# Optimization experiments

Hardware: AMD Instinct MI355X
Metric: run time of the kernel (lower is better)

## Reference

```python
import jax, jax.numpy as jnp
import numpy as np

NUM_GAUSSIANS = 3  # coordinate dims per spot; nfeatures = 2*NG + 1 = 7


def setup_inputs() -> dict:
    key = jax.random.key(0)
    k1, k2 = jax.random.split(key)
    # uniform [0,1) keeps prob/sigma channels positive (module clamps anyway)
    features = jax.random.uniform(k1, (16, 16, 7, 64, 64), dtype=jnp.float32)
    targets = jax.random.uniform(k2, (16, 16, 32, 4), dtype=jnp.float32)
    return {"features": features, "targets": targets}


def reference(features, targets):
    ng = NUM_GAUSSIANS
    B, F, nf, h, w = features.shape
    max_spots = targets.shape[2]

    feat = features.reshape(-1, nf, h, w)             # (BF, 7, h, w)
    tgt = targets.reshape(-1, max_spots, ng + 1)      # (BF, S, ng+1)
    mask = tgt[..., 0]                                # (BF, S)
    true_values = tgt[..., 1:]                        # (BF, S, ng)

    prob = jnp.clip(feat[:, 0], 1e-20).reshape(-1, h * w)              # (BF, hw)
    mu = feat[:, 1:ng + 1].reshape(-1, ng, h * w)                      # (BF, ng, hw)
    sigma = jnp.clip(feat[:, 1 + ng:], 1e-10).reshape(-1, ng, h * w)   # (BF, ng, hw)

    logprob_norm = jnp.log(prob) - jnp.log(prob.sum(-1, keepdims=True))  # (BF, hw)

    # broadcast: (BF, S, ng, 1) vs (BF, 1, ng, hw) -> (BF, S, ng, hw)
    inputs = true_values[:, :, :, None]
    means = mu[:, None]
    sigmas = sigma[:, None]
    log_normal = -(inputs - means) ** 2 / (2.0 * sigmas ** 2) - jnp.log(sigmas)

    # sum over gaussian dims, logsumexp over spatial mixture components
    log_gmm_prob = jax.nn.logsumexp(logprob_norm[:, None] + log_normal.sum(2), axis=2)  # (BF, S)

    loss_gmm = jnp.sum(log_gmm_prob * mask, axis=-1)  # (BF,)
    return (-loss_gmm).reshape(B, F)
```

## Files before the change

### kernel.cpp

```cpp
#include <hip/hip_runtime.h>

#define NG 3
#define HW 4096
#define NSPOT 32
#define NSPLIT 4
#define PXB (HW / NSPLIT)
#define TPB 256
#define PXT (PXB / TPB)

#define HALF_LOG2E 0.7213475204444817f
#define LN2 0.6931471805599453f

__device__ __forceinline__ float wave_reduce_sum(float v) {
#pragma unroll
    for (int m = 1; m < 64; m <<= 1) v += __shfl_xor(v, m, 64);
    return v;
}

__global__ __launch_bounds__(TPB) void gmm_main(const float* __restrict__ feat,
                                                const float* __restrict__ tgt,
                                                float* __restrict__ wsS,
                                                float* __restrict__ wsP) {
    const int b = blockIdx.x >> 2;
    const int slice = blockIdx.x & 3;
    const int tid = threadIdx.x;
    const int lane = tid & 63;
    const int wv = tid >> 6;

    __shared__ float spot_tab[NSPOT][8];
    __shared__ float Ssh[4][NSPOT];
    __shared__ float Psh[4];

    if (tid < NSPOT) {
        const float* tb = tgt + (size_t)b * (NSPOT * 4) + tid * 4;
        float t0 = tb[1], t1 = tb[2], t2 = tb[3];
        spot_tab[tid][0] = t0 * t0;
        spot_tab[tid][1] = t1 * t1;
        spot_tab[tid][2] = t2 * t2;
        spot_tab[tid][3] = 0.f;
        spot_tab[tid][4] = -2.f * t0;
        spot_tab[tid][5] = -2.f * t1;
        spot_tab[tid][6] = -2.f * t2;
        spot_tab[tid][7] = 0.f;
    }
    __syncthreads();

    const float* fb = feat + (size_t)b * (7 * HW) + slice * PXB;
    const int p4 = tid * 4;

    float4 f0 = *(const float4*)(fb + 0 * HW + p4);
    float4 f1 = *(const float4*)(fb + 1 * HW + p4);
    float4 f2 = *(const float4*)(fb + 2 * HW + p4);
    float4 f3 = *(const float4*)(fb + 3 * HW + p4);
    float4 f4v = *(const float4*)(fb + 4 * HW + p4);
    float4 f5 = *(const float4*)(fb + 5 * HW + p4);
    float4 f6 = *(const float4*)(fb + 6 * HW + p4);

    float pr[PXT] = {f0.x, f0.y, f0.z, f0.w};
    float mu[NG][PXT] = {{f1.x, f1.y, f1.z, f1.w},
                         {f2.x, f2.y, f2.z, f2.w},
                         {f3.x, f3.y, f3.z, f3.w}};
    float sg[NG][PXT] = {{f4v.x, f4v.y, f4v.z, f4v.w},
                         {f5.x, f5.y, f5.z, f5.w},
                         {f6.x, f6.y, f6.z, f6.w}};

    float A[NG][PXT], Bc[NG][PXT], C[PXT];
    float psum = 0.f;
#pragma unroll
    for (int k = 0; k < PXT; ++k) {
        float p = fmaxf(pr[k], 1e-20f);
        psum += p;
        float c2 = __builtin_amdgcn_logf(p);
#pragma unroll
        for (int g = 0; g < NG; ++g) {
            float s = fmaxf(sg[g][k], 1e-10f);
            c2 -= __builtin_amdgcn_logf(s);
            float nis = -HALF_LOG2E * __builtin_amdgcn_rcpf(s * s);
            float m = mu[g][k];
            A[g][k] = nis;
            Bc[g][k] = m * nis;
            c2 = fmaf(m * m, nis, c2);
        }
        C[k] = c2;
    }

#pragma unroll
    for (int s = 0; s < NSPOT; ++s) {
        float4 tsq = *(const float4*)&spot_tab[s][0];
        float4 tq = *(const float4*)&spot_tab[s][4];
        float acc = 0.f;
#pragma unroll
        for (int k = 0; k < PXT; ++k) {
            float x = C[k];
            x = fmaf(tsq.x, A[0][k], x);
            x = fmaf(tsq.y, A[1][k], x);
            x = fmaf(tsq.z, A[2][k], x);
            x = fmaf(tq.x, Bc[0][k], x);
            x = fmaf(tq.y, Bc[1][k], x);
            x = fmaf(tq.z, Bc[2][k], x);
            acc += __builtin_amdgcn_exp2f(x);
        }
        float r = wave_reduce_sum(acc);
        if (lane == 0) Ssh[wv][s] = r;
    }
    float rp = wave_reduce_sum(psum);
    if (lane == 0) Psh[wv] = rp;
    __syncthreads();

    if (tid < NSPOT) {
        float tot = Ssh[0][tid] + Ssh[1][tid] + Ssh[2][tid] + Ssh[3][tid];
        atomicAdd(&wsS[b * NSPOT + tid], tot);
    }
    if (tid == 0) {
        atomicAdd(&wsP[b], Psh[0] + Psh[1] + Psh[2] + Psh[3]);
    }
}

__global__ __launch_bounds__(64) void gmm_final(const float* __restrict__ tgt,
                                                const float* __restrict__ wsS,
                                                const float* __restrict__ wsP,
                                                float* __restrict__ out) {
    int b = blockIdx.x * blockDim.x + threadIdx.x;
    if (b >= 256) return;
    float lp = __builtin_amdgcn_logf(wsP[b]) * LN2;
    float acc = 0.f;
#pragma unroll 4
    for (int s = 0; s < NSPOT; ++s) {
        float mask = tgt[(size_t)b * 128 + s * 4];
        float ls = __builtin_amdgcn_logf(wsS[b * NSPOT + s]) * LN2;
        acc = fmaf(mask, ls - lp, acc);
    }
    out[b] = -acc;
}

extern "C" void kernel_launch(void* const* d_in, const int* in_sizes, int n_in,
                              void* d_out, int out_size, void* d_ws, size_t ws_size,
                              hipStream_t stream) {
    const float* feat = (const float*)d_in[0];
    const float* tgt = (const float*)d_in[1];
    float* out = (float*)d_out;

    float* wsS = (float*)d_ws;
    float* wsP = wsS + 256 * NSPOT;

    hipMemsetAsync(d_ws, 0, (256 * NSPOT + 256) * sizeof(float), stream);

    gmm_main<<<256 * NSPLIT, TPB, 0, stream>>>(feat, tgt, wsS, wsP);
    gmm_final<<<4, 64, 0, stream>>>(tgt, wsS, wsP, out);
}
```

Baseline: 90.15 us.

## Pack math in float2, transpose-reduce spots, drop memset and atomics

The spot loop now uses 2-wide float vectors on (t-mu)^2*a, which may let the compiler emit packed FP32 instructions, and it drops the precomputed A/B/C expansion. The 32 per-spot wave reductions become a butterfly transpose-reduce that needs far fewer shuffles. Per-slice partials are written directly instead of via atomics, which removes the hipMemsetAsync launch. The final kernel is parallelised to one wave per batch. The trade-offs are a larger per-thread accumulator array and a slightly different floating-point summation order.

```diff
diff --git a/kernel.cpp b/kernel.cpp
--- a/kernel.cpp
+++ b/kernel.cpp
@@ -2,20 +2,19 @@
 
 #define NG 3
 #define HW 4096
+#define NB 256
 #define NSPOT 32
 #define NSPLIT 4
 #define PXB (HW / NSPLIT)
 #define TPB 256
 #define PXT (PXB / TPB)
+#define NPAIR (PXT / 2)
+#define NWAVE (TPB / 64)
 
-#define HALF_LOG2E 0.7213475204444817f
+#define NHALF_LOG2E -0.7213475204444817f
 #define LN2 0.6931471805599453f
 
-__device__ __forceinline__ float wave_reduce_sum(float v) {
-#pragma unroll
-    for (int m = 1; m < 64; m <<= 1) v += __shfl_xor(v, m, 64);
-    return v;
-}
+typedef float f32x2 __attribute__((ext_vector_type(2)));
 
 __global__ __launch_bounds__(TPB) void gmm_main(const float* __restrict__ feat,
                                                 const float* __restrict__ tgt,
@@ -27,21 +26,13 @@
     const int lane = tid & 63;
     const int wv = tid >> 6;
 
-    __shared__ float spot_tab[NSPOT][8];
-    __shared__ float Ssh[4][NSPOT];
-    __shared__ float Psh[4];
+    __shared__ float4 spot_tab[NSPOT];
+    __shared__ float Ssh[NWAVE][NSPOT];
+    __shared__ float Psh[NWAVE];
 
     if (tid < NSPOT) {
         const float* tb = tgt + (size_t)b * (NSPOT * 4) + tid * 4;
-        float t0 = tb[1], t1 = tb[2], t2 = tb[3];
-        spot_tab[tid][0] = t0 * t0;
-        spot_tab[tid][1] = t1 * t1;
-        spot_tab[tid][2] = t2 * t2;
-        spot_tab[tid][3] = 0.f;
-        spot_tab[tid][4] = -2.f * t0;
-        spot_tab[tid][5] = -2.f * t1;
-        spot_tab[tid][6] = -2.f * t2;
-        spot_tab[tid][7] = 0.f;
+        spot_tab[tid] = make_float4(tb[1], tb[2], tb[3], 0.f);
     }
     __syncthreads();
 
@@ -57,14 +48,14 @@
     float4 f6 = *(const float4*)(fb + 6 * HW + p4);
 
     float pr[PXT] = {f0.x, f0.y, f0.z, f0.w};
-    float mu[NG][PXT] = {{f1.x, f1.y, f1.z, f1.w},
-                         {f2.x, f2.y, f2.z, f2.w},
-                         {f3.x, f3.y, f3.z, f3.w}};
-    float sg[NG][PXT] = {{f4v.x, f4v.y, f4v.z, f4v.w},
-                         {f5.x, f5.y, f5.z, f5.w},
-                         {f6.x, f6.y, f6.z, f6.w}};
+    float mu_s[NG][PXT] = {{f1.x, f1.y, f1.z, f1.w},
+                           {f2.x, f2.y, f2.z, f2.w},
+                           {f3.x, f3.y, f3.z, f3.w}};
+    float sg_s[NG][PXT] = {{f4v.x, f4v.y, f4v.z, f4v.w},
+                           {f5.x, f5.y, f5.z, f5.w},
+                           {f6.x, f6.y, f6.z, f6.w}};
 
-    float A[NG][PXT], Bc[NG][PXT], C[PXT];
+    float a_s[NG][PXT], c_s[PXT];
     float psum = 0.f;
 #pragma unroll
     for (int k = 0; k < PXT; ++k) {
@@ -73,46 +64,86 @@
         float c2 = __builtin_amdgcn_logf(p);
 #pragma unroll
         for (int g = 0; g < NG; ++g) {
-            float s = fmaxf(sg[g][k], 1e-10f);
+            float s = fmaxf(sg_s[g][k], 1e-10f);
             c2 -= __builtin_amdgcn_logf(s);
-            float nis = -HALF_LOG2E * __builtin_amdgcn_rcpf(s * s);
-            float m = mu[g][k];
-            A[g][k] = nis;
-            Bc[g][k] = m * nis;
-            c2 = fmaf(m * m, nis, c2);
+            a_s[g][k] = NHALF_LOG2E * __builtin_amdgcn_rcpf(s * s);
         }
-        C[k] = c2;
+        c_s[k] = c2;
     }
 
+    f32x2 MU[NG][NPAIR], A[NG][NPAIR], C[NPAIR];
+#pragma unroll
+    for (int pp = 0; pp < NPAIR; ++pp) {
+        C[pp] = (f32x2){c_s[2 * pp], c_s[2 * pp + 1]};
+#pragma unroll
+        for (int g = 0; g < NG; ++g) {
+            MU[g][pp] = (f32x2){mu_s[g][2 * pp], mu_s[g][2 * pp + 1]};
+            A[g][pp] = (f32x2){a_s[g][2 * pp], a_s[g][2 * pp + 1]};
+        }
+    }
+
+    float acc[NSPOT];
 #pragma unroll
     for (int s = 0; s < NSPOT; ++s) {
-        float4 tsq = *(const float4*)&spot_tab[s][0];
-        float4 tq = *(const float4*)&spot_tab[s][4];
-        float acc = 0.f;
+        float4 t = spot_tab[s];
+        f32x2 x[NPAIR];
 #pragma unroll
-        for (int k = 0; k < PXT; ++k) {
-            float x = C[k];
-            x = fmaf(tsq.x, A[0][k], x);
-            x = fmaf(tsq.y, A[1][k], x);
-            x = fmaf(tsq.z, A[2][k], x);
-            x = fmaf(tq.x, Bc[0][k], x);
-            x = fmaf(tq.y, Bc[1][k], x);
-            x = fmaf(tq.z, Bc[2][k], x);
-            acc += __builtin_amdgcn_exp2f(x);
+        for (int pp = 0; pp < NPAIR; ++pp) {
+            f32x2 x2 = C[pp];
+            {
+                f32x2 z = t.x - MU[0][pp];
+                x2 += (z * A[0][pp]) * z;
+            }
+            {
+                f32x2 z = t.y - MU[1][pp];
+                x2 += (z * A[1][pp]) * z;
+            }
+            {
+                f32x2 z = t.z - MU[2][pp];
+                x2 += (z * A[2][pp]) * z;
+            }
+            x[pp] = x2;
         }
-        float r = wave_reduce_sum(acc);
-        if (lane == 0) Ssh[wv][s] = r;
+        float e0 = __builtin_amdgcn_exp2f(x[0].x) + __builtin_amdgcn_exp2f(x[0].y);
+        float e1 = __builtin_amdgcn_exp2f(x[1].x) + __builtin_amdgcn_exp2f(x[1].y);
+        acc[s] = e0 + e1;
     }
-    float rp = wave_reduce_sum(psum);
-    if (lane == 0) Psh[wv] = rp;
+
+#define RSTEP(D, HALF)                                          \
+    {                                                           \
+        const bool hi = (lane & (D)) != 0;                      \
+        _Pragma("unroll") for (int i = 0; i < (HALF); ++i) {    \
+            float send = hi ? acc[i] : acc[i + (HALF)];         \
+            float recv = __shfl_xor(send, (D), 64);             \
+            acc[i] = (hi ? acc[i + (HALF)] : acc[i]) + recv;    \
+        }                                                       \
+    }
+    RSTEP(32, 16)
+    RSTEP(16, 8)
+    RSTEP(8, 4)
+    RSTEP(4, 2)
+    RSTEP(2, 1)
+#undef RSTEP
+    acc[0] += __shfl_xor(acc[0], 1, 64);
+    if ((lane & 1) == 0) Ssh[wv][lane >> 1] = acc[0];
+
+    float ps = psum;
+#pragma unroll
+    for (int m = 1; m < 64; m <<= 1) ps += __shfl_xor(ps, m, 64);
+    if (lane == 0) Psh[wv] = ps;
     __syncthreads();
 
     if (tid < NSPOT) {
-        float tot = Ssh[0][tid] + Ssh[1][tid] + Ssh[2][tid] + Ssh[3][tid];
-        atomicAdd(&wsS[b * NSPOT + tid], tot);
+        float tot = 0.f;
+#pragma unroll
+        for (int w = 0; w < NWAVE; ++w) tot += Ssh[w][tid];
+        wsS[((size_t)b * NSPLIT + slice) * NSPOT + tid] = tot;
     }
-    if (tid == 0) {
-        atomicAdd(&wsP[b], Psh[0] + Psh[1] + Psh[2] + Psh[3]);
+    if (tid == NSPOT) {
+        float tot = 0.f;
+#pragma unroll
+        for (int w = 0; w < NWAVE; ++w) tot += Psh[w];
+        wsP[b * NSPLIT + slice] = tot;
     }
 }
 
@@ -120,17 +151,26 @@
                                                 const float* __restrict__ wsS,
                                                 const float* __restrict__ wsP,
                                                 float* __restrict__ out) {
-    int b = blockIdx.x * blockDim.x + threadIdx.x;
-    if (b >= 256) return;
-    float lp = __builtin_amdgcn_logf(wsP[b]) * LN2;
-    float acc = 0.f;
-#pragma unroll 4
-    for (int s = 0; s < NSPOT; ++s) {
-        float mask = tgt[(size_t)b * 128 + s * 4];
-        float ls = __builtin_amdgcn_logf(wsS[b * NSPOT + s]) * LN2;
-        acc = fmaf(mask, ls - lp, acc);
+    const int b = blockIdx.x;
+    const int lane = threadIdx.x;
+
+    float ps = (lane < NSPLIT) ? wsP[b * NSPLIT + lane] : 0.f;
+#pragma unroll
+    for (int m = 1; m < 64; m <<= 1) ps += __shfl_xor(ps, m, 64);
+
+    float contrib = 0.f;
+    if (lane < NSPOT) {
+        float S = 0.f;
+#pragma unroll
+        for (int k = 0; k < NSPLIT; ++k)
+            S += wsS[((size_t)b * NSPLIT + k) * NSPOT + lane];
+        float mask = tgt[(size_t)b * (NSPOT * 4) + lane * 4];
+        contrib = mask * (__builtin_amdgcn_logf(S) - __builtin_amdgcn_logf(ps));
     }
-    out[b] = -acc;
+#pragma unroll
+    for (int m = 1; m < 64; m <<= 1) contrib += __shfl_xor(contrib, m, 64);
+
+    if (lane == 0) out[b] = -contrib * LN2;
 }
 
 extern "C" void kernel_launch(void* const* d_in, const int* in_sizes, int n_in,
@@ -141,10 +181,8 @@
     float* out = (float*)d_out;
 
     float* wsS = (float*)d_ws;
-    float* wsP = wsS + 256 * NSPOT;
+    float* wsP = wsS + NB * NSPLIT * NSPOT;
 
-    hipMemsetAsync(d_ws, 0, (256 * NSPOT + 256) * sizeof(float), stream);
-
-    gmm_main<<<256 * NSPLIT, TPB, 0, stream>>>(feat, tgt, wsS, wsP);
-    gmm_final<<<4, 64, 0, stream>>>(tgt, wsS, wsP, out);
+    gmm_main<<<NB * NSPLIT, TPB, 0, stream>>>(feat, tgt, wsS, wsP);
+    gmm_final<<<NB, 64, 0, stream>>>(tgt, wsS, wsP, out);
 }
```

Result: faster. 82.94 us (-8.0%).
